# Kernel tuning notes

Hardware: AMD Instinct MI355X
Metric: run time of the kernel (lower is better)

The kernel has to match this reference:

```python
import jax, jax.numpy as jnp
import numpy as np

IN_FEATURES = 4096
OUT_FEATURES = 4096
ALPHA = 0.01  # dequant scale = input_scale * weight_scale
BETA = 1.0


def setup_inputs() -> dict:
    key = jax.random.key(0)
    kx, kw, kb = jax.random.split(key, 3)
    # int8 activations (W8A8): values in [-127, 127]
    x = jax.random.randint(kx, (4, 2048, IN_FEATURES), -127, 128, dtype=jnp.int8)
    # int8 weight buffer, [out_features, in_features] as in the torch module
    weight = jax.random.randint(kw, (OUT_FEATURES, IN_FEATURES), -127, 128, dtype=jnp.int8)
    # fp32 bias, [1, out_features]
    bias = jax.random.normal(kb, (1, OUT_FEATURES), dtype=jnp.float32)
    alpha = jnp.float32(ALPHA)
    return {"x": x, "weight": weight, "bias": bias, "alpha": alpha}


def reference(x, weight, bias, alpha):
    # y = alpha * (x_int8 @ W_int8^T) + beta * bias, accumulated in int32, output fp32
    x_shape = x.shape
    x2 = x.reshape(-1, x_shape[-1])  # [B*S, in]
    # int8 GEMM with int32 accumulation (faithful to the fused kernel's math)
    acc = jax.lax.dot_general(
        x2, weight,
        dimension_numbers=(((1,), (1,)), ((), ())),
        preferred_element_type=jnp.int32,
    )  # [B*S, out]
    y = alpha * acc.astype(jnp.float32) + BETA * bias  # fused dequant + bias
    return y.reshape(*x_shape[:-1], OUT_FEATURES)
```

## Files before the change

### kernel.cpp

```cpp
#include <hip/hip_runtime.h>
#include <stdint.h>

typedef int v4i __attribute__((ext_vector_type(4)));

constexpr int K_DIM = 4096;
constexpr int N_DIM = 4096;
constexpr int TM = 128;
constexpr int TN = 128;
constexpr int TK = 128;
constexpr int KSTEPS = K_DIM / TK;

__device__ __forceinline__ int pack4(int a, int b, int c, int d) {
    unsigned r = (unsigned(a) & 0xFFu)
               | ((unsigned(b) & 0xFFu) << 8)
               | ((unsigned(c) & 0xFFu) << 16)
               | (unsigned(d) << 24);
    return (int)r;
}

__global__ __launch_bounds__(256) void pack_both(
    const int* __restrict__ s1, int* __restrict__ d1, int n1,
    const int* __restrict__ s2, int* __restrict__ d2, int n2)
{
    int idx = blockIdx.x * blockDim.x + threadIdx.x;
    const int* s;
    int* d;
    if (idx < n1) { s = s1; d = d1; }
    else if (idx < n1 + n2) { s = s2; d = d2; idx -= n1; }
    else return;
    v4i v = ((const v4i*)s)[idx];
    d[idx] = pack4(v.x, v.y, v.z, v.w);
}

__device__ __forceinline__ void gld16(const int8_t* g, int8_t* l) {
    __builtin_amdgcn_global_load_lds(
        (const __attribute__((address_space(1))) char*)g,
        (__attribute__((address_space(3))) char*)l,
        16, 0, 0);
}

constexpr int BM = 256;
constexpr int BN = 256;
constexpr int HKB = 64;
constexpr int NH = K_DIM / HKB;

__global__ __launch_bounds__(512, 2) void w8a8_gemm_256p(
    const int8_t* __restrict__ X,
    const int8_t* __restrict__ Wt,
    const float*  __restrict__ bias,
    const float*  __restrict__ alphap,
    float* __restrict__ Y)
{
    extern __shared__ __align__(128) int8_t smem[];

    const int tid  = threadIdx.x;
    const int lane = tid & 63;
    const int wave = tid >> 6;

    const int flat = blockIdx.x;
    const int swz  = (flat & 7) * 64 + (flat >> 3);
    const int m0   = (swz & 31) * BM;
    const int n0   = (swz >> 5) * BN;

    int ga[2], gb[2], ls[2];
#pragma unroll
    for (int q = 0; q < 2; ++q) {
        const int c   = q * 512 + tid;
        const int row = c >> 2;
        const int sl  = ((c & 3) ^ ((row >> 1) & 3)) << 4;
        ga[q] = (m0 + row) * K_DIM + sl;
        gb[q] = (n0 + row) * K_DIM + sl;
        ls[q] = c << 4;
    }

    const int wm   = (wave & 1) << 7;
    const int wn   = (wave >> 1) << 6;
    const int lrow = lane & 15;
    const int quad = lane >> 4;

    int a_off[8], b_off[4];
#pragma unroll
    for (int i = 0; i < 8; ++i) {
        const int ra = wm + i * 16 + lrow;
        a_off[i] = ra * HKB + ((quad ^ ((ra >> 1) & 3)) << 4);
    }
#pragma unroll
    for (int j = 0; j < 4; ++j) {
        const int rb = wn + j * 16 + lrow;
        b_off[j] = 16384 + rb * HKB + ((quad ^ ((rb >> 1) & 3)) << 4);
    }

    v4i acc[8][4] = {};

#pragma unroll
    for (int p = 0; p < 3; ++p) {
        int8_t* ib = smem + (p << 15);
        const int kb = p * HKB;
        gld16(X  + ga[0] + kb, ib + ls[0]);
        gld16(X  + ga[1] + kb, ib + ls[1]);
        gld16(Wt + gb[0] + kb, ib + 16384 + ls[0]);
        gld16(Wt + gb[1] + kb, ib + 16384 + ls[1]);
    }

#define KHALF_BODY(VMN, DOISS)                                               \
    {                                                                        \
        asm volatile("s_waitcnt vmcnt(" #VMN ")" ::: "memory");              \
        __builtin_amdgcn_s_barrier();                                        \
        int8_t* Ab = smem + ((h & 3) << 15);                                 \
        if (DOISS) {                                                         \
            int8_t* ib  = smem + (((h + 3) & 3) << 15);                      \
            const int k3 = (h + 3) * HKB;                                    \
            gld16(X + ga[0] + k3, ib + ls[0]);                               \
            gld16(X + ga[1] + k3, ib + ls[1]);                               \
        }                                                                    \
        v4i a[8], b[4];                                                      \
        _Pragma("unroll")                                                    \
        for (int i = 0; i < 4; ++i) a[i] = *(const v4i*)(Ab + a_off[i]);     \
        _Pragma("unroll")                                                    \
        for (int j = 0; j < 4; ++j) b[j] = *(const v4i*)(Ab + b_off[j]);     \
        __builtin_amdgcn_s_setprio(1);                                       \
        _Pragma("unroll")                                                    \
        for (int i = 0; i < 4; ++i)                                          \
            _Pragma("unroll")                                                \
            for (int j = 0; j < 4; ++j)                                      \
                acc[i][j] = __builtin_amdgcn_mfma_i32_16x16x64_i8(           \
                    a[i], b[j], acc[i][j], 0, 0, 0);                         \
        __builtin_amdgcn_s_setprio(0);                                       \
        if (DOISS) {                                                         \
            int8_t* ib  = smem + (((h + 3) & 3) << 15);                      \
            const int k3 = (h + 3) * HKB;                                    \
            gld16(Wt + gb[0] + k3, ib + 16384 + ls[0]);                      \
            gld16(Wt + gb[1] + k3, ib + 16384 + ls[1]);                      \
        }                                                                    \
        _Pragma("unroll")                                                    \
        for (int i = 4; i < 8; ++i) a[i] = *(const v4i*)(Ab + a_off[i]);     \
        __builtin_amdgcn_s_setprio(1);                                       \
        _Pragma("unroll")                                                    \
        for (int i = 4; i < 8; ++i)                                          \
            _Pragma("unroll")                                                \
            for (int j = 0; j < 4; ++j)                                      \
                acc[i][j] = __builtin_amdgcn_mfma_i32_16x16x64_i8(           \
                    a[i], b[j], acc[i][j], 0, 0, 0);                         \
        __builtin_amdgcn_s_setprio(0);                                       \
    }

#pragma unroll 1
    for (int h = 0; h < 61; ++h) KHALF_BODY(8, true)
    { const int h = 61; KHALF_BODY(8, false) }
    { const int h = 62; KHALF_BODY(4, false) }
    { const int h = 63; KHALF_BODY(0, false) }
#undef KHALF_BODY

    const float alpha = *alphap;
#pragma unroll
    for (int j = 0; j < 4; ++j) {
        const int col = n0 + wn + j * 16 + lrow;
        const float bj = bias[col];
#pragma unroll
        for (int i = 0; i < 8; ++i) {
            const size_t rbase = (size_t)(m0 + wm + i * 16 + quad * 4) * N_DIM + col;
#pragma unroll
            for (int r = 0; r < 4; ++r)
                Y[rbase + (size_t)r * N_DIM] = fmaf(alpha, (float)acc[i][j][r], bj);
        }
    }
}

__global__ __launch_bounds__(256) void w8a8_gemm_packed(
    const int8_t* __restrict__ X,
    const int8_t* __restrict__ Wt,
    const float*  __restrict__ bias,
    const float*  __restrict__ alphap,
    float* __restrict__ Y)
{
    __shared__ __align__(16) int8_t As[TM * TK];
    __shared__ __align__(16) int8_t Bs[TN * TK];

    const int tid  = threadIdx.x;
    const int lane = tid & 63;
    const int wave = tid >> 6;

    const int m0 = blockIdx.x * TM;
    const int n0 = blockIdx.y * TN;

    const int8_t* Aga[4];
    const int8_t* Bga[4];
    int lds_off[4];
#pragma unroll
    for (int i = 0; i < 4; ++i) {
        const int c    = (wave * 4 + i) * 64 + lane;
        const int row  = c >> 3;
        const int gko  = ((c & 7) ^ ((row >> 1) & 7)) << 4;
        Aga[i] = X  + (size_t)(m0 + row) * K_DIM + gko;
        Bga[i] = Wt + (size_t)(n0 + row) * K_DIM + gko;
        lds_off[i] = c << 4;
    }

    const int wm   = (wave & 1) << 6;
    const int wn   = (wave >> 1) << 6;
    const int lrow = lane & 15;
    const int quad = lane >> 4;

    int a_off[4], b_off[4];
#pragma unroll
    for (int i = 0; i < 4; ++i) {
        const int ra = wm + i * 16 + lrow;
        a_off[i] = ra * TK + ((quad ^ ((ra >> 1) & 7)) << 4);
        const int rb = wn + i * 16 + lrow;
        b_off[i] = rb * TK + ((quad ^ ((rb >> 1) & 7)) << 4);
    }

    v4i acc[4][4] = {};

    for (int kt = 0; kt < KSTEPS; ++kt) {
        const int kb = kt * TK;
#pragma unroll
        for (int i = 0; i < 4; ++i) {
            gld16(Aga[i] + kb, As + lds_off[i]);
            gld16(Bga[i] + kb, Bs + lds_off[i]);
        }
        __syncthreads();

#pragma unroll
        for (int kk = 0; kk < 2; ++kk) {
            const int kx = kk << 6;
            v4i a[4], b[4];
#pragma unroll
            for (int i = 0; i < 4; ++i) a[i] = *(const v4i*)(As + (a_off[i] ^ kx));
#pragma unroll
            for (int j = 0; j < 4; ++j) b[j] = *(const v4i*)(Bs + (b_off[j] ^ kx));
#pragma unroll
            for (int i = 0; i < 4; ++i)
#pragma unroll
                for (int j = 0; j < 4; ++j)
                    acc[i][j] = __builtin_amdgcn_mfma_i32_16x16x64_i8(a[i], b[j], acc[i][j], 0, 0, 0);
        }

        __syncthreads();
    }

    const float alpha = *alphap;
#pragma unroll
    for (int j = 0; j < 4; ++j) {
        const int col = n0 + wn + j * 16 + lrow;
        const float bj = bias[col];
#pragma unroll
        for (int i = 0; i < 4; ++i) {
            const size_t rbase = (size_t)(m0 + wm + i * 16 + quad * 4) * N_DIM + col;
#pragma unroll
            for (int r = 0; r < 4; ++r)
                Y[rbase + (size_t)r * N_DIM] = fmaf(alpha, (float)acc[i][j][r], bj);
        }
    }
}

__global__ __launch_bounds__(256, 2) void w8a8_gemm_fb(
    const int*   __restrict__ X,
    const int*   __restrict__ Wt,
    const float* __restrict__ bias,
    const float* __restrict__ alphap,
    float* __restrict__ Y)
{
    __shared__ __align__(16) int8_t As[TM * 64];
    __shared__ __align__(16) int8_t Bs[TN * 64];

    const int tid  = threadIdx.x;
    const int lane = tid & 63;
    const int wave = tid >> 6;
    const int m0 = blockIdx.x * TM;
    const int n0 = blockIdx.y * TN;

    const int srow = tid >> 3;
    const int sk   = (tid & 7) * 8;
    const int* Ag = X  + (size_t)(m0 + srow) * K_DIM + sk;
    const int* Bg = Wt + (size_t)(n0 + srow) * K_DIM + sk;

    int wr_off[4];
#pragma unroll
    for (int r = 0; r < 4; ++r) {
        const int row = r * 32 + (tid >> 3);
        const int dw  = (tid & 7) * 2;
        const int sw  = row * 16 + (((dw >> 2) ^ ((row >> 1) & 3)) << 2) + (dw & 3);
        wr_off[r] = sw * 4;
    }

    const int wm   = (wave & 1) << 6;
    const int wn   = (wave >> 1) << 6;
    const int lrow = lane & 15;
    const int quad = lane >> 4;

    int a_off[4], b_off[4];
#pragma unroll
    for (int i = 0; i < 4; ++i) {
        const int ra = wm + i * 16 + lrow;
        a_off[i] = ra * 64 + ((quad ^ ((ra >> 1) & 3)) << 4);
        const int rb = wn + i * 16 + lrow;
        b_off[i] = rb * 64 + ((quad ^ ((rb >> 1) & 3)) << 4);
    }

    v4i acc[4][4] = {};
    v4i av[8], bv[8];
#pragma unroll
    for (int r = 0; r < 4; ++r) {
        const int* pa = Ag + (size_t)r * 32 * K_DIM;
        const int* pb = Bg + (size_t)r * 32 * K_DIM;
        av[2 * r] = *(const v4i*)(pa);  av[2 * r + 1] = *(const v4i*)(pa + 4);
        bv[2 * r] = *(const v4i*)(pb);  bv[2 * r + 1] = *(const v4i*)(pb + 4);
    }

    for (int kt = 0; kt < 64; ++kt) {
#pragma unroll
        for (int r = 0; r < 4; ++r) {
            int2 pa2, pb2;
            pa2.x = pack4(av[2*r].x,   av[2*r].y,   av[2*r].z,   av[2*r].w);
            pa2.y = pack4(av[2*r+1].x, av[2*r+1].y, av[2*r+1].z, av[2*r+1].w);
            pb2.x = pack4(bv[2*r].x,   bv[2*r].y,   bv[2*r].z,   bv[2*r].w);
            pb2.y = pack4(bv[2*r+1].x, bv[2*r+1].y, bv[2*r+1].z, bv[2*r+1].w);
            *(int2*)(As + wr_off[r]) = pa2;
            *(int2*)(Bs + wr_off[r]) = pb2;
        }
        const int kn = (kt + 1 < 64) ? (kt + 1) : kt;
        const int koff = kn * 64;
#pragma unroll
        for (int r = 0; r < 4; ++r) {
            const int* pa = Ag + (size_t)r * 32 * K_DIM + koff;
            const int* pb = Bg + (size_t)r * 32 * K_DIM + koff;
            av[2 * r] = *(const v4i*)(pa);  av[2 * r + 1] = *(const v4i*)(pa + 4);
            bv[2 * r] = *(const v4i*)(pb);  bv[2 * r + 1] = *(const v4i*)(pb + 4);
        }
        __syncthreads();
        v4i a[4], b[4];
#pragma unroll
        for (int i = 0; i < 4; ++i) a[i] = *(const v4i*)(As + a_off[i]);
#pragma unroll
        for (int j = 0; j < 4; ++j) b[j] = *(const v4i*)(Bs + b_off[j]);
#pragma unroll
        for (int i = 0; i < 4; ++i)
#pragma unroll
            for (int j = 0; j < 4; ++j)
                acc[i][j] = __builtin_amdgcn_mfma_i32_16x16x64_i8(a[i], b[j], acc[i][j], 0, 0, 0);
        __syncthreads();
    }

    const float alpha = *alphap;
#pragma unroll
    for (int j = 0; j < 4; ++j) {
        const int col = n0 + wn + j * 16 + lrow;
        const float bj = bias[col];
#pragma unroll
        for (int i = 0; i < 4; ++i) {
            const size_t rbase = (size_t)(m0 + wm + i * 16 + quad * 4) * N_DIM + col;
#pragma unroll
            for (int r = 0; r < 4; ++r)
                Y[rbase + (size_t)r * N_DIM] = fmaf(alpha, (float)acc[i][j][r], bj);
        }
    }
}

extern "C" void kernel_launch(void* const* d_in, const int* in_sizes, int n_in,
                              void* d_out, int out_size, void* d_ws, size_t ws_size,
                              hipStream_t stream) {
    const int*   X32   = (const int*)d_in[0];
    const int*   W32   = (const int*)d_in[1];
    const float* bias  = (const float*)d_in[2];
    const float* alpha = (const float*)d_in[3];
    float* Y = (float*)d_out;

    const int nX = in_sizes[0];
    const int nW = in_sizes[1];
    const int M  = nX / K_DIM;

    if (ws_size >= (size_t)nX + (size_t)nW) {
        int8_t* Xp = (int8_t*)d_ws;
        int8_t* Wp = Xp + nX;
        const int n1 = nX / 4, n2 = nW / 4;
        const int nthreads = n1 + n2;
        pack_both<<<(nthreads + 255) / 256, 256, 0, stream>>>(
            X32, (int*)Xp, n1, W32, (int*)Wp, n2);

        static hipError_t attr = hipFuncSetAttribute(
            reinterpret_cast<const void*>(w8a8_gemm_256p),
            hipFuncAttributeMaxDynamicSharedMemorySize, 131072);

        if (attr == hipSuccess && (M % BM) == 0) {
            const int nblocks = (M / BM) * (N_DIM / BN);
            w8a8_gemm_256p<<<dim3(nblocks), dim3(512), 131072, stream>>>(
                Xp, Wp, bias, alpha, Y);
        } else {
            dim3 grid(M / TM, N_DIM / TN);
            w8a8_gemm_packed<<<grid, dim3(256), 0, stream>>>(Xp, Wp, bias, alpha, Y);
        }
    } else {
        dim3 grid(M / TM, N_DIM / TN);
        w8a8_gemm_fb<<<grid, dim3(256), 0, stream>>>(X32, W32, bias, alpha, Y);
    }
}
```

Before: 388.5 us.

## Double-buffer A fragments in registers and move the barrier to the end of each K-step

The main loop is software-pipelined so that each K-half step first loads the B fragments and issues all four global-to-LDS loads for stage h+3. It then prefetches the next stage's A fragments into an alternate register set (aE/aO ping-pong) before running all 32 MFMAs on the current A registers. The vmcnt wait and barrier move to the tail of each step, and a sched_barrier pins the ordering. The aim is to hide LDS read latency behind the MFMA work and cut barrier stalls at the top of each step. The cost is 16 extra live vector registers for A, which risks spills or lower occupancy under the 512-thread, 2-block launch bound.

New measurement: 397.8 us. +2.4%, slower.

```diff
diff --git a/kernel.cpp b/kernel.cpp
--- a/kernel.cpp
+++ b/kernel.cpp
@@ -44,7 +44,7 @@
 constexpr int HKB = 64;
 constexpr int NH = K_DIM / HKB;
 
-__global__ __launch_bounds__(512, 2) void w8a8_gemm_256p(
+__global__ __launch_bounds__(512, 2) void w8a8_gemm_256s(
     const int8_t* __restrict__ X,
     const int8_t* __restrict__ Wt,
     const float*  __restrict__ bias,
@@ -91,6 +91,7 @@
     }
 
     v4i acc[8][4] = {};
+    v4i aE[8], aO[8], b[4];
 
 #pragma unroll
     for (int p = 0; p < 3; ++p) {
@@ -101,54 +102,54 @@
         gld16(Wt + gb[0] + kb, ib + 16384 + ls[0]);
         gld16(Wt + gb[1] + kb, ib + 16384 + ls[1]);
     }
-
-#define KHALF_BODY(VMN, DOISS)                                               \
+    asm volatile("s_waitcnt vmcnt(4)" ::: "memory");
+    __builtin_amdgcn_s_barrier();
+#pragma unroll
+    for (int i = 0; i < 8; ++i) aE[i] = *(const v4i*)(smem + a_off[i]);
+
+#define KHALF_BODY(H, CUR, NXT, ISS, AN, TAIL, VMSTR)                        \
     {                                                                        \
-        asm volatile("s_waitcnt vmcnt(" #VMN ")" ::: "memory");              \
-        __builtin_amdgcn_s_barrier();                                        \
-        int8_t* Ab = smem + ((h & 3) << 15);                                 \
-        if (DOISS) {                                                         \
-            int8_t* ib  = smem + (((h + 3) & 3) << 15);                      \
-            const int k3 = (h + 3) * HKB;                                    \
-            gld16(X + ga[0] + k3, ib + ls[0]);                               \
-            gld16(X + ga[1] + k3, ib + ls[1]);                               \
+        const int h_ = (H);                                                  \
+        int8_t* Ub = smem + ((h_ & 3) << 15);                                \
+        _Pragma("unroll")                                                    \
+        for (int j = 0; j < 4; ++j) b[j] = *(const v4i*)(Ub + b_off[j]);     \
+        if (ISS) {                                                           \
+            int8_t* ib  = smem + (((h_ + 3) & 3) << 15);                     \
+            const int k3 = (h_ + 3) * HKB;                                   \
+            gld16(X  + ga[0] + k3, ib + ls[0]);                              \
+            gld16(X  + ga[1] + k3, ib + ls[1]);                              \
+            gld16(Wt + gb[0] + k3, ib + 16384 + ls[0]);                      \
+            gld16(Wt + gb[1] + k3, ib + 16384 + ls[1]);                      \
         }                                                                    \
-        v4i a[8], b[4];                                                      \
-        _Pragma("unroll")                                                    \
-        for (int i = 0; i < 4; ++i) a[i] = *(const v4i*)(Ab + a_off[i]);     \
-        _Pragma("unroll")                                                    \
-        for (int j = 0; j < 4; ++j) b[j] = *(const v4i*)(Ab + b_off[j]);     \
+        if (AN) {                                                            \
+            int8_t* Nb = smem + (((h_ + 1) & 3) << 15);                      \
+            _Pragma("unroll")                                                \
+            for (int i = 0; i < 8; ++i) NXT[i] = *(const v4i*)(Nb + a_off[i]); \
+        }                                                                    \
+        __builtin_amdgcn_sched_barrier(0);                                   \
         __builtin_amdgcn_s_setprio(1);                                       \
         _Pragma("unroll")                                                    \
-        for (int i = 0; i < 4; ++i)                                          \
+        for (int i = 0; i < 8; ++i)                                          \
             _Pragma("unroll")                                                \
             for (int j = 0; j < 4; ++j)                                      \
                 acc[i][j] = __builtin_amdgcn_mfma_i32_16x16x64_i8(           \
-                    a[i], b[j], acc[i][j], 0, 0, 0);                         \
+                    CUR[i], b[j], acc[i][j], 0, 0, 0);                       \
         __builtin_amdgcn_s_setprio(0);                                       \
-        if (DOISS) {                                                         \
-            int8_t* ib  = smem + (((h + 3) & 3) << 15);                      \
-            const int k3 = (h + 3) * HKB;                                    \
-            gld16(Wt + gb[0] + k3, ib + 16384 + ls[0]);                      \
-            gld16(Wt + gb[1] + k3, ib + 16384 + ls[1]);                      \
+        if (TAIL) {                                                          \
+            asm volatile(VMSTR ::: "memory");                                \
+            __builtin_amdgcn_s_barrier();                                    \
         }                                                                    \
-        _Pragma("unroll")                                                    \
-        for (int i = 4; i < 8; ++i) a[i] = *(const v4i*)(Ab + a_off[i]);     \
-        __builtin_amdgcn_s_setprio(1);                                       \
-        _Pragma("unroll")                                                    \
-        for (int i = 4; i < 8; ++i)                                          \
-            _Pragma("unroll")                                                \
-            for (int j = 0; j < 4; ++j)                                      \
-                acc[i][j] = __builtin_amdgcn_mfma_i32_16x16x64_i8(           \
-                    a[i], b[j], acc[i][j], 0, 0, 0);                         \
-        __builtin_amdgcn_s_setprio(0);                                       \
     }
 
 #pragma unroll 1
-    for (int h = 0; h < 61; ++h) KHALF_BODY(8, true)
-    { const int h = 61; KHALF_BODY(8, false) }
-    { const int h = 62; KHALF_BODY(4, false) }
-    { const int h = 63; KHALF_BODY(0, false) }
+    for (int h = 0; h < 60; h += 2) {
+        KHALF_BODY(h,     aE, aO, true, true, true, "s_waitcnt vmcnt(4)")
+        KHALF_BODY(h + 1, aO, aE, true, true, true, "s_waitcnt vmcnt(4)")
+    }
+    KHALF_BODY(60, aE, aO, true,  true,  true,  "s_waitcnt vmcnt(4)")
+    KHALF_BODY(61, aO, aE, false, true,  true,  "s_waitcnt vmcnt(0)")
+    KHALF_BODY(62, aE, aO, false, true,  true,  "s_waitcnt vmcnt(0)")
+    KHALF_BODY(63, aO, aE, false, false, false, "")
 #undef KHALF_BODY
 
     const float alpha = *alphap;
@@ -379,12 +380,12 @@
             X32, (int*)Xp, n1, W32, (int*)Wp, n2);
 
         static hipError_t attr = hipFuncSetAttribute(
-            reinterpret_cast<const void*>(w8a8_gemm_256p),
+            reinterpret_cast<const void*>(w8a8_gemm_256s),
             hipFuncAttributeMaxDynamicSharedMemorySize, 131072);
 
         if (attr == hipSuccess && (M % BM) == 0) {
             const int nblocks = (M / BM) * (N_DIM / BN);
-            w8a8_gemm_256p<<<dim3(nblocks), dim3(512), 131072, stream>>>(
+            w8a8_gemm_256s<<<dim3(nblocks), dim3(512), 131072, stream>>>(
                 Xp, Wp, bias, alpha, Y);
         } else {
             dim3 grid(M / TM, N_DIM / TN);
```
